# Kernel tuning notes

Hardware: AMD Instinct MI355X
Metric: run time of the kernel (lower is better)

The kernel has to match this reference:

```python
import jax, jax.numpy as jnp
import numpy as np

BIG = 1000000.0


def setup_inputs() -> dict:
    key = jax.random.key(0)
    k1, k2 = jax.random.split(key)
    embeddings = jax.random.normal(k1, (8192, 128), dtype=jnp.float32)
    labels = jax.random.randint(k2, (8192,), 0, 512, dtype=jnp.int64)
    return {"embeddings": embeddings, "labels": labels, "margin": jnp.float32(0.5)}


def _pairwise_euclidean(x):
    # [N, N] Euclidean distance matrix, numerically safe sqrt (zero diag)
    sq = jnp.sum(x * x, axis=1)
    d2 = sq[:, None] + sq[None, :] - 2.0 * (x @ x.T)
    d2 = jnp.maximum(d2, 0.0)
    nz = d2 > 0.0
    return jnp.where(nz, jnp.sqrt(jnp.where(nz, d2, 1.0)), 0.0)


def reference(embeddings, labels, margin):
    n = embeddings.shape[0]
    dist = _pairwise_euclidean(embeddings)                      # [N, N]
    same = (labels[:, None] == labels[None, :]).astype(dist.dtype)
    mask_pos = same - jnp.eye(n, dtype=dist.dtype)              # positives, excl. self
    mask_neg = 1.0 - same                                       # different label
    pos_dist = jnp.max(dist * mask_pos, axis=1)                 # hardest positive
    neg_dist = jnp.min(dist + (1.0 - mask_neg) * BIG, axis=1)   # hardest negative
    loss = jax.nn.relu(pos_dist - neg_dist + margin)
    return jnp.mean(loss)
```

## Files before the change

kernel.cpp:

```cpp
#include <hip/hip_runtime.h>
#include <hip/hip_bf16.h>

#define NROW 8192
#define DIM  128
#define JSPLIT 8
#define BIGF 1e30f

typedef __attribute__((ext_vector_type(8))) short bf16x8;
typedef __attribute__((ext_vector_type(4))) float f32x4;


__device__ __forceinline__ unsigned short f2bf(float f) {
    unsigned u = __float_as_uint(f);
    unsigned r = (u + 0x7fffu + ((u >> 16) & 1u)) >> 16;
    return (unsigned short)r;
}

__global__ __launch_bounds__(256) void prep_kernel(const float* __restrict__ x,
                                                   const int* __restrict__ lbl,
                                                   unsigned short* __restrict__ xbT,
                                                   uint2* __restrict__ meta,
                                                   unsigned* __restrict__ posb,
                                                   unsigned* __restrict__ negb,
                                                   float* __restrict__ out) {
    int gtid = blockIdx.x * 256 + threadIdx.x;
    if (gtid < NROW) {
        posb[gtid] = 0u;
        negb[gtid] = __float_as_uint(BIGF);
    }
    if (gtid == 0) out[0] = 0.0f;

    int wave = gtid >> 6;
    int lane = threadIdx.x & 63;
    int q = lane >> 4, l = lane & 15;
    int row = wave * 16 + l;
    const float* xr = x + (size_t)row * DIM + q * 8;

    float s = 0.0f;
    #pragma unroll
    for (int ks = 0; ks < 4; ks++) {
        float4 a = *(const float4*)(xr + ks * 32);
        float4 b = *(const float4*)(xr + ks * 32 + 4);
        s += a.x * a.x + a.y * a.y + a.z * a.z + a.w * a.w;
        s += b.x * b.x + b.y * b.y + b.z * b.z + b.w * b.w;
        uint4 u;
        u.x = (unsigned)f2bf(a.x) | ((unsigned)f2bf(a.y) << 16);
        u.y = (unsigned)f2bf(a.z) | ((unsigned)f2bf(a.w) << 16);
        u.z = (unsigned)f2bf(b.x) | ((unsigned)f2bf(b.y) << 16);
        u.w = (unsigned)f2bf(b.z) | ((unsigned)f2bf(b.w) << 16);
        *(uint4*)(xbT + (size_t)wave * 2048 + ks * 512 + lane * 8) = u;
    }
    s += __shfl_xor(s, 16);
    s += __shfl_xor(s, 32);
    if (q == 0) {
        uint2 mv;
        mv.x = __float_as_uint(s);
        mv.y = (unsigned)lbl[row];
        meta[row] = mv;
    }
}

__global__ __launch_bounds__(256, 2) void tri_mfma(const unsigned short* __restrict__ xbT,
                                                   const uint2* __restrict__ meta,
                                                   unsigned* __restrict__ posb,
                                                   unsigned* __restrict__ negb) {
    const int bid  = blockIdx.x;
    const int rb   = bid >> 3;
    const int jq   = bid & 7;
    const int i0   = rb * 128;
    const int t    = threadIdx.x;
    const int lane = t & 63;
    const int w    = t >> 6;
    const int wrow = (w >> 1) * 64;
    const int wcol = (w & 1) * 64;
    const int quad = lane >> 4;
    const int l15  = lane & 15;

    bf16x8 A[4][4];
    {
        const int tbase = (i0 + wrow) >> 4;
        #pragma unroll
        for (int ti = 0; ti < 4; ti++)
            #pragma unroll
            for (int ks = 0; ks < 4; ks++)
                A[ti][ks] = *(const bf16x8*)(xbT + ((size_t)(tbase + ti) * 2048 + ks * 512 + lane * 8));
    }

    float sqi[4][4]; int lbli[4][4];
    #pragma unroll
    for (int ti = 0; ti < 4; ti++) {
        int rbase = i0 + wrow + ti * 16 + quad * 4;
        uint4 m01 = *(const uint4*)(meta + rbase);
        uint4 m23 = *(const uint4*)(meta + rbase + 2);
        sqi[ti][0] = __uint_as_float(m01.x); lbli[ti][0] = (int)m01.y;
        sqi[ti][1] = __uint_as_float(m01.z); lbli[ti][1] = (int)m01.w;
        sqi[ti][2] = __uint_as_float(m23.x); lbli[ti][2] = (int)m23.y;
        sqi[ti][3] = __uint_as_float(m23.z); lbli[ti][3] = (int)m23.w;
    }

    float posm[4][4], negm[4][4];
    #pragma unroll
    for (int ti = 0; ti < 4; ti++)
        #pragma unroll
        for (int r = 0; r < 4; r++) { posm[ti][r] = -BIGF; negm[ti][r] = BIGF; }

    const int jbase = jq * (NROW / JSPLIT);
    const int dr    = l15 - quad * 4;

    #pragma unroll 1
    for (int jt = 0; jt < (NROW / JSPLIT) / 128; jt++) {
        const int j0 = jbase + jt * 128;
        const int tb = (j0 + wcol) >> 4;

        bf16x8 Bv[4][4];
        #pragma unroll
        for (int tj = 0; tj < 4; tj++)
            #pragma unroll
            for (int ks = 0; ks < 4; ks++)
                Bv[tj][ks] = *(const bf16x8*)(xbT + ((size_t)(tb + tj) * 2048 + ks * 512 + lane * 8));

        float sqj[4]; int lblj[4];
        #pragma unroll
        for (int tj = 0; tj < 4; tj++) {
            uint2 mv = meta[j0 + wcol + tj * 16 + l15];
            sqj[tj]  = __uint_as_float(mv.x);
            lblj[tj] = (int)mv.y;
        }

        f32x4 acc[4][4];
        #pragma unroll
        for (int ti = 0; ti < 4; ti++)
            #pragma unroll
            for (int tj = 0; tj < 4; tj++) acc[ti][tj] = (f32x4){0.f, 0.f, 0.f, 0.f};

        #pragma unroll
        for (int ks = 0; ks < 4; ks++)
            #pragma unroll
            for (int ti = 0; ti < 4; ti++)
                #pragma unroll
                for (int tj = 0; tj < 4; tj++)
                    acc[ti][tj] = __builtin_amdgcn_mfma_f32_16x16x32_bf16(A[ti][ks], Bv[tj][ks], acc[ti][tj], 0, 0, 0);

        const bool diag = (i0 + wrow) == (j0 + wcol);
        if (!diag) {
            #pragma unroll
            for (int ti = 0; ti < 4; ti++)
                #pragma unroll
                for (int tj = 0; tj < 4; tj++)
                    #pragma unroll
                    for (int r = 0; r < 4; r++) {
                        float s = fmaf(-2.0f, acc[ti][tj][r], sqj[tj]);
                        bool same = (lbli[ti][r] == lblj[tj]);
                        posm[ti][r] = fmaxf(posm[ti][r], same ? s : -BIGF);
                        negm[ti][r] = fminf(negm[ti][r], same ? BIGF : s);
                    }
        } else {
            #pragma unroll
            for (int ti = 0; ti < 4; ti++)
                #pragma unroll
                for (int tj = 0; tj < 4; tj++)
                    #pragma unroll
                    for (int r = 0; r < 4; r++) {
                        float s = fmaf(-2.0f, acc[ti][tj][r], sqj[tj]);
                        bool same = (lbli[ti][r] == lblj[tj]);
                        bool isd  = (ti == tj) && (dr == r);
                        posm[ti][r] = fmaxf(posm[ti][r], (same && !isd) ? s : -BIGF);
                        negm[ti][r] = fminf(negm[ti][r], same ? BIGF : s);
                    }
        }
    }

    #pragma unroll
    for (int ti = 0; ti < 4; ti++)
        #pragma unroll
        for (int r = 0; r < 4; r++) {
            float p = posm[ti][r];
            float n = negm[ti][r];
            #pragma unroll
            for (int m = 8; m >= 1; m >>= 1) {
                p = fmaxf(p, __shfl_xor(p, m));
                n = fminf(n, __shfl_xor(n, m));
            }
            if (l15 == 0) {
                int row = i0 + wrow + ti * 16 + quad * 4 + r;
                float d2p = fmaxf(0.0f, sqi[ti][r] + p);
                float d2n = fmaxf(0.0f, sqi[ti][r] + n);
                atomicMax(&posb[row], __float_as_uint(d2p));
                atomicMin(&negb[row], __float_as_uint(d2n));
            }
        }
}

__global__ __launch_bounds__(256) void tri_final(const unsigned* __restrict__ posb,
                                                 const unsigned* __restrict__ negb,
                                                 const float* __restrict__ margin,
                                                 float* __restrict__ out) {
    int r = blockIdx.x * 256 + threadIdx.x;
    float m = margin[0];
    float p  = sqrtf(__uint_as_float(posb[r]));
    float ng = sqrtf(__uint_as_float(negb[r]));
    float loss = fmaxf(p - ng + m, 0.0f) * (1.0f / (float)NROW);
    #pragma unroll
    for (int o = 32; o > 0; o >>= 1) loss += __shfl_down(loss, o);
    __shared__ float wsum[4];
    int lane = threadIdx.x & 63, wv = threadIdx.x >> 6;
    if (lane == 0) wsum[wv] = loss;
    __syncthreads();
    if (threadIdx.x == 0) atomicAdd(out, wsum[0] + wsum[1] + wsum[2] + wsum[3]);
}

extern "C" void kernel_launch(void* const* d_in, const int* in_sizes, int n_in,
                              void* d_out, int out_size, void* d_ws, size_t ws_size,
                              hipStream_t stream) {
    const float* x      = (const float*)d_in[0];
    const int*   lbl    = (const int*)d_in[1];
    const float* margin = (const float*)d_in[2];
    float* out = (float*)d_out;

    unsigned short* xbT = (unsigned short*)d_ws;
    uint2*    meta = (uint2*)((char*)d_ws + (size_t)NROW * DIM * 2);
    unsigned* posb = (unsigned*)((char*)meta + NROW * 8);
    unsigned* negb = posb + NROW;

    prep_kernel<<<128, 256, 0, stream>>>(x, lbl, xbT, meta, posb, negb, out);
    tri_mfma<<<64 * JSPLIT, 256, 0, stream>>>(xbT, meta, posb, negb);
    tri_final<<<NROW / 256, 256, 0, stream>>>(posb, negb, margin, out);
}
```

Measured before the change: 93.06 us.

## Fold -2 scale and norms into MFMA, fuse final reduction via last-block counter

```diff
diff --git a/kernel.cpp b/kernel.cpp
--- a/kernel.cpp
+++ b/kernel.cpp
@@ -3,7 +3,7 @@
 
 #define NROW 8192
 #define DIM  128
-#define JSPLIT 8
+#define NBLK 512
 #define BIGF 1e30f
 
 typedef __attribute__((ext_vector_type(8))) short bf16x8;
@@ -12,58 +12,79 @@
 
 __device__ __forceinline__ unsigned short f2bf(float f) {
     unsigned u = __float_as_uint(f);
-    unsigned r = (u + 0x7fffu + ((u >> 16) & 1u)) >> 16;
-    return (unsigned short)r;
+    return (unsigned short)((u + 0x7fffu + ((u >> 16) & 1u)) >> 16);
 }
 
 __global__ __launch_bounds__(256) void prep_kernel(const float* __restrict__ x,
                                                    const int* __restrict__ lbl,
                                                    unsigned short* __restrict__ xbT,
+                                                   unsigned short* __restrict__ xbM2,
                                                    uint2* __restrict__ meta,
                                                    unsigned* __restrict__ posb,
                                                    unsigned* __restrict__ negb,
+                                                   unsigned* __restrict__ counter,
                                                    float* __restrict__ out) {
-    int gtid = blockIdx.x * 256 + threadIdx.x;
-    if (gtid < NROW) {
-        posb[gtid] = 0u;
-        negb[gtid] = __float_as_uint(BIGF);
-    }
-    if (gtid == 0) out[0] = 0.0f;
-
-    int wave = gtid >> 6;
-    int lane = threadIdx.x & 63;
-    int q = lane >> 4, l = lane & 15;
-    int row = wave * 16 + l;
-    const float* xr = x + (size_t)row * DIM + q * 8;
+    __shared__ unsigned short Al[32][136];
+    __shared__ unsigned short Ml[32][136];
+    __shared__ float sqp[32][8];
+
+    const int b = blockIdx.x, t = threadIdx.x;
+    const int gid = b * 256 + t;
+    if (gid < NROW) { posb[gid] = 0u; negb[gid] = __float_as_uint(BIGF); }
+    if (gid == 0)   { counter[0] = 0u; out[0] = 0.0f; }
+
+    const int R0  = b * 32;
+    const int r   = t >> 3;
+    const int seg = t & 7;
+    const float* src = x + (size_t)(R0 + r) * DIM + seg * 16;
 
     float s = 0.0f;
     #pragma unroll
-    for (int ks = 0; ks < 4; ks++) {
-        float4 a = *(const float4*)(xr + ks * 32);
-        float4 b = *(const float4*)(xr + ks * 32 + 4);
-        s += a.x * a.x + a.y * a.y + a.z * a.z + a.w * a.w;
-        s += b.x * b.x + b.y * b.y + b.z * b.z + b.w * b.w;
-        uint4 u;
-        u.x = (unsigned)f2bf(a.x) | ((unsigned)f2bf(a.y) << 16);
-        u.y = (unsigned)f2bf(a.z) | ((unsigned)f2bf(a.w) << 16);
-        u.z = (unsigned)f2bf(b.x) | ((unsigned)f2bf(b.y) << 16);
-        u.w = (unsigned)f2bf(b.z) | ((unsigned)f2bf(b.w) << 16);
-        *(uint4*)(xbT + (size_t)wave * 2048 + ks * 512 + lane * 8) = u;
-    }
-    s += __shfl_xor(s, 16);
-    s += __shfl_xor(s, 32);
-    if (q == 0) {
+    for (int c4 = 0; c4 < 4; c4++) {
+        float4 v = *(const float4*)(src + c4 * 4);
+        s += v.x * v.x + v.y * v.y + v.z * v.z + v.w * v.w;
+        uint2 ua, um;
+        ua.x = (unsigned)f2bf(v.x) | ((unsigned)f2bf(v.y) << 16);
+        ua.y = (unsigned)f2bf(v.z) | ((unsigned)f2bf(v.w) << 16);
+        um.x = (unsigned)f2bf(-2.0f * v.x) | ((unsigned)f2bf(-2.0f * v.y) << 16);
+        um.y = (unsigned)f2bf(-2.0f * v.z) | ((unsigned)f2bf(-2.0f * v.w) << 16);
+        *(uint2*)&Al[r][seg * 16 + c4 * 4] = ua;
+        *(uint2*)&Ml[r][seg * 16 + c4 * 4] = um;
+    }
+    sqp[r][seg] = s;
+    __syncthreads();
+
+    if (t < 32) {
+        float ss = 0.0f;
+        #pragma unroll
+        for (int q = 0; q < 8; q++) ss += sqp[t][q];
         uint2 mv;
-        mv.x = __float_as_uint(s);
-        mv.y = (unsigned)lbl[row];
-        meta[row] = mv;
+        mv.x = __float_as_uint(ss);
+        mv.y = (unsigned)lbl[R0 + t];
+        meta[R0 + t] = mv;
+    }
+
+    const int ks = t >> 6, lane = t & 63;
+    const int q = lane >> 4, l = lane & 15;
+    #pragma unroll
+    for (int tl = 0; tl < 2; tl++) {
+        int row = tl * 16 + l, col = ks * 32 + q * 8;
+        uint4 va = *(const uint4*)&Al[row][col];
+        uint4 vm = *(const uint4*)&Ml[row][col];
+        size_t off = (size_t)(R0 / 16 + tl) * 2048 + ks * 512 + lane * 8;
+        *(uint4*)(xbT  + off) = va;
+        *(uint4*)(xbM2 + off) = vm;
     }
 }
 
 __global__ __launch_bounds__(256, 2) void tri_mfma(const unsigned short* __restrict__ xbT,
+                                                   const unsigned short* __restrict__ xbM2,
                                                    const uint2* __restrict__ meta,
                                                    unsigned* __restrict__ posb,
-                                                   unsigned* __restrict__ negb) {
+                                                   unsigned* __restrict__ negb,
+                                                   unsigned* __restrict__ counter,
+                                                   const float* __restrict__ margin,
+                                                   float* __restrict__ out) {
     const int bid  = blockIdx.x;
     const int rb   = bid >> 3;
     const int jq   = bid & 7;
@@ -104,20 +125,14 @@
         #pragma unroll
         for (int r = 0; r < 4; r++) { posm[ti][r] = -BIGF; negm[ti][r] = BIGF; }
 
-    const int jbase = jq * (NROW / JSPLIT);
+    const int jbase = jq * (NROW / 8);
     const int dr    = l15 - quad * 4;
 
     #pragma unroll 1
-    for (int jt = 0; jt < (NROW / JSPLIT) / 128; jt++) {
+    for (int jt = 0; jt < 8; jt++) {
         const int j0 = jbase + jt * 128;
         const int tb = (j0 + wcol) >> 4;
-
-        bf16x8 Bv[4][4];
-        #pragma unroll
-        for (int tj = 0; tj < 4; tj++)
-            #pragma unroll
-            for (int ks = 0; ks < 4; ks++)
-                Bv[tj][ks] = *(const bf16x8*)(xbT + ((size_t)(tb + tj) * 2048 + ks * 512 + lane * 8));
+        const bool diag = (i0 + wrow) == (j0 + wcol);
 
         float sqj[4]; int lblj[4];
         #pragma unroll
@@ -127,46 +142,46 @@
             lblj[tj] = (int)mv.y;
         }
 
-        f32x4 acc[4][4];
-        #pragma unroll
-        for (int ti = 0; ti < 4; ti++)
-            #pragma unroll
-            for (int tj = 0; tj < 4; tj++) acc[ti][tj] = (f32x4){0.f, 0.f, 0.f, 0.f};
-
-        #pragma unroll
-        for (int ks = 0; ks < 4; ks++)
+        #pragma unroll
+        for (int tj = 0; tj < 4; tj++) {
+            bf16x8 Bv[4];
+            #pragma unroll
+            for (int ks = 0; ks < 4; ks++)
+                Bv[ks] = *(const bf16x8*)(xbM2 + ((size_t)(tb + tj) * 2048 + ks * 512 + lane * 8));
+
+            f32x4 acc[4];
             #pragma unroll
             for (int ti = 0; ti < 4; ti++)
+                acc[ti] = (f32x4){sqj[tj], sqj[tj], sqj[tj], sqj[tj]};
+
+            #pragma unroll
+            for (int ks = 0; ks < 4; ks++)
                 #pragma unroll
-                for (int tj = 0; tj < 4; tj++)
-                    acc[ti][tj] = __builtin_amdgcn_mfma_f32_16x16x32_bf16(A[ti][ks], Bv[tj][ks], acc[ti][tj], 0, 0, 0);
-
-        const bool diag = (i0 + wrow) == (j0 + wcol);
-        if (!diag) {
-            #pragma unroll
-            for (int ti = 0; ti < 4; ti++)
+                for (int ti = 0; ti < 4; ti++)
+                    acc[ti] = __builtin_amdgcn_mfma_f32_16x16x32_bf16(A[ti][ks], Bv[ks], acc[ti], 0, 0, 0);
+
+            if (!diag) {
                 #pragma unroll
-                for (int tj = 0; tj < 4; tj++)
+                for (int ti = 0; ti < 4; ti++)
                     #pragma unroll
                     for (int r = 0; r < 4; r++) {
-                        float s = fmaf(-2.0f, acc[ti][tj][r], sqj[tj]);
+                        float s = acc[ti][r];
                         bool same = (lbli[ti][r] == lblj[tj]);
                         posm[ti][r] = fmaxf(posm[ti][r], same ? s : -BIGF);
                         negm[ti][r] = fminf(negm[ti][r], same ? BIGF : s);
                     }
-        } else {
-            #pragma unroll
-            for (int ti = 0; ti < 4; ti++)
+            } else {
                 #pragma unroll
-                for (int tj = 0; tj < 4; tj++)
+                for (int ti = 0; ti < 4; ti++)
                     #pragma unroll
                     for (int r = 0; r < 4; r++) {
-                        float s = fmaf(-2.0f, acc[ti][tj][r], sqj[tj]);
+                        float s = acc[ti][r];
                         bool same = (lbli[ti][r] == lblj[tj]);
                         bool isd  = (ti == tj) && (dr == r);
                         posm[ti][r] = fmaxf(posm[ti][r], (same && !isd) ? s : -BIGF);
                         negm[ti][r] = fminf(negm[ti][r], same ? BIGF : s);
                     }
+            }
         }
     }
 
@@ -189,24 +204,33 @@
                 atomicMin(&negb[row], __float_as_uint(d2n));
             }
         }
-}
-
-__global__ __launch_bounds__(256) void tri_final(const unsigned* __restrict__ posb,
-                                                 const unsigned* __restrict__ negb,
-                                                 const float* __restrict__ margin,
-                                                 float* __restrict__ out) {
-    int r = blockIdx.x * 256 + threadIdx.x;
-    float m = margin[0];
-    float p  = sqrtf(__uint_as_float(posb[r]));
-    float ng = sqrtf(__uint_as_float(negb[r]));
-    float loss = fmaxf(p - ng + m, 0.0f) * (1.0f / (float)NROW);
-    #pragma unroll
-    for (int o = 32; o > 0; o >>= 1) loss += __shfl_down(loss, o);
+
+    __threadfence();
+    __shared__ unsigned lastflag;
     __shared__ float wsum[4];
-    int lane = threadIdx.x & 63, wv = threadIdx.x >> 6;
-    if (lane == 0) wsum[wv] = loss;
     __syncthreads();
-    if (threadIdx.x == 0) atomicAdd(out, wsum[0] + wsum[1] + wsum[2] + wsum[3]);
+    if (t == 0) {
+        unsigned prev = __hip_atomic_fetch_add(counter, 1u, __ATOMIC_ACQ_REL, __HIP_MEMORY_SCOPE_AGENT);
+        lastflag = (prev == NBLK - 1) ? 1u : 0u;
+    }
+    __syncthreads();
+    if (lastflag) {
+        __threadfence();
+        float mg = margin[0];
+        float loss = 0.0f;
+        for (int row = t; row < NROW; row += 256) {
+            unsigned pb = __hip_atomic_load(&posb[row], __ATOMIC_RELAXED, __HIP_MEMORY_SCOPE_AGENT);
+            unsigned nb = __hip_atomic_load(&negb[row], __ATOMIC_RELAXED, __HIP_MEMORY_SCOPE_AGENT);
+            float p  = sqrtf(__uint_as_float(pb));
+            float ng = sqrtf(__uint_as_float(nb));
+            loss += fmaxf(p - ng + mg, 0.0f);
+        }
+        #pragma unroll
+        for (int o = 32; o > 0; o >>= 1) loss += __shfl_down(loss, o);
+        if (lane == 0) wsum[w] = loss;
+        __syncthreads();
+        if (t == 0) out[0] = (wsum[0] + wsum[1] + wsum[2] + wsum[3]) * (1.0f / (float)NROW);
+    }
 }
 
 extern "C" void kernel_launch(void* const* d_in, const int* in_sizes, int n_in,
@@ -217,12 +241,14 @@
     const float* margin = (const float*)d_in[2];
     float* out = (float*)d_out;
 
-    unsigned short* xbT = (unsigned short*)d_ws;
-    uint2*    meta = (uint2*)((char*)d_ws + (size_t)NROW * DIM * 2);
+    const size_t MAT = (size_t)NROW * DIM * 2;
+    unsigned short* xbT  = (unsigned short*)d_ws;
+    unsigned short* xbM2 = (unsigned short*)((char*)d_ws + MAT);
+    uint2*    meta = (uint2*)((char*)d_ws + 2 * MAT);
     unsigned* posb = (unsigned*)((char*)meta + NROW * 8);
     unsigned* negb = posb + NROW;
-
-    prep_kernel<<<128, 256, 0, stream>>>(x, lbl, xbT, meta, posb, negb, out);
-    tri_mfma<<<64 * JSPLIT, 256, 0, stream>>>(xbT, meta, posb, negb);
-    tri_final<<<NROW / 256, 256, 0, stream>>>(posb, negb, margin, out);
-}
+    unsigned* counter = negb + NROW;
+
+    prep_kernel<<<NROW / 32, 256, 0, stream>>>(x, lbl, xbT, xbM2, meta, posb, negb, counter, out);
+    tri_mfma<<<NBLK, 256, 0, stream>>>(xbT, xbM2, meta, posb, negb, counter, margin, out);
+}
```

New measurement: 136.5 us. 46.7% more time.
